# Kernel tuning notes

Measured on AMD Instinct MI355X. Metric: run time of the kernel, lower is better.

Reference implementation:

```python
import jax, jax.numpy as jnp
import numpy as np

B, S, H, L, NH, F, V, K, R = 64, 512, 256, 4, 8, 1024, 50265, 8, 25
DH = H // NH
EPS = 1e-5


def layernorm(x, g, b):
    mu = x.mean(-1, keepdims=True)
    var = ((x - mu) ** 2).mean(-1, keepdims=True)
    return (x - mu) * jax.lax.rsqrt(var + EPS) * g + b


def setup_inputs() -> dict:
    key = jax.random.key(0)
    ks = jax.random.split(key, 24)
    input_ids = jax.random.randint(ks[0], (B, S), 0, V, dtype=jnp.int64)
    # prefix attention mask with variable valid lengths (ragged sequences)
    lengths = jax.random.randint(ks[1], (B,), 16, S + 1)
    attention_mask = (jnp.arange(S)[None, :] < lengths[:, None]).astype(jnp.int32)
    sub_indices = jax.random.randint(ks[2], (B, K), 0, S, dtype=jnp.int64)
    obj_indices = jax.random.randint(ks[3], (B, K), 0, S, dtype=jnp.int64)
    sub_counts = jax.random.randint(ks[4], (B,), 0, K + 1, dtype=jnp.int32)
    obj_counts = jax.random.randint(ks[5], (B,), 0, K + 1, dtype=jnp.int32)
    sc = 0.02
    p = {
        'emb': jax.random.normal(ks[6], (V, H), jnp.float32) * sc,
        'Wqkv': jax.random.normal(ks[7], (L, H, 3 * H), jnp.float32) * sc,
        'bqkv': jnp.zeros((L, 3 * H), jnp.float32),
        'Wo': jax.random.normal(ks[8], (L, H, H), jnp.float32) * sc,
        'bo': jnp.zeros((L, H), jnp.float32),
        'ln1_g': jnp.ones((L, H), jnp.float32), 'ln1_b': jnp.zeros((L, H), jnp.float32),
        'ln2_g': jnp.ones((L, H), jnp.float32), 'ln2_b': jnp.zeros((L, H), jnp.float32),
        'W1': jax.random.normal(ks[9], (L, H, F), jnp.float32) * sc,
        'b1': jnp.zeros((L, F), jnp.float32),
        'W2': jax.random.normal(ks[10], (L, F, H), jnp.float32) * sc,
        'b2': jnp.zeros((L, H), jnp.float32),
        'lnf_g': jnp.ones((H,), jnp.float32), 'lnf_b': jnp.zeros((H,), jnp.float32),
        'mW1': jax.random.normal(ks[11], (3 * H, H), jnp.float32) * sc,
        'mb1': jnp.zeros((H,), jnp.float32),
        'mW2': jax.random.normal(ks[12], (H, R), jnp.float32) * sc,
        'mb2': jnp.zeros((R,), jnp.float32),
    }
    return dict(input_ids=input_ids, attention_mask=attention_mask,
                sub_indices=sub_indices, sub_counts=sub_counts,
                obj_indices=obj_indices, obj_counts=obj_counts, **p)


def _encoder(input_ids, attention_mask, emb, Wqkv, bqkv, Wo, bo,
             ln1_g, ln1_b, ln2_g, ln2_b, W1, b1, W2, b2, lnf_g, lnf_b):
    x = emb[input_ids]  # [B,S,H]
    kbias = jnp.where(attention_mask[:, None, None, :] > 0, 0.0, -1e9)  # mask keys
    scale = 1.0 / np.sqrt(DH)
    for l in range(L):  # small fixed layer loop
        qkv = x @ Wqkv[l] + bqkv[l]
        q, k, v = jnp.split(qkv, 3, axis=-1)
        q = q.reshape(B, S, NH, DH).transpose(0, 2, 1, 3)
        k = k.reshape(B, S, NH, DH).transpose(0, 2, 1, 3)
        v = v.reshape(B, S, NH, DH).transpose(0, 2, 1, 3)
        scores = jnp.einsum('bhqd,bhkd->bhqk', q, k) * scale + kbias
        attn = jax.nn.softmax(scores, axis=-1)
        o = jnp.einsum('bhqk,bhkd->bhqd', attn, v).transpose(0, 2, 1, 3).reshape(B, S, H)
        x = layernorm(x + o @ Wo[l] + bo[l], ln1_g[l], ln1_b[l])
        h = jax.nn.relu(x @ W1[l] + b1[l]) @ W2[l] + b2[l]
        x = layernorm(x + h, ln2_g[l], ln2_b[l])
    return layernorm(x, lnf_g, lnf_b)


def _pooled(seq, idx, counts):
    g = jnp.take_along_axis(seq, idx[:, :, None], axis=1)  # [B,K,H]
    m = (jnp.arange(K)[None, :] < counts[:, None]).astype(seq.dtype)
    s = (g * m[:, :, None]).sum(1)
    c = counts.astype(seq.dtype)[:, None]
    return jnp.where(c > 0, s / jnp.maximum(c, 1.0), 0.0)  # zeros if no indices


def reference(input_ids, attention_mask, sub_indices, sub_counts, obj_indices, obj_counts,
              emb, Wqkv, bqkv, Wo, bo, ln1_g, ln1_b, ln2_g, ln2_b,
              W1, b1, W2, b2, lnf_g, lnf_b, mW1, mb1, mW2, mb2):
    seq = _encoder(input_ids, attention_mask, emb, Wqkv, bqkv, Wo, bo,
                   ln1_g, ln1_b, ln2_g, ln2_b, W1, b1, W2, b2, lnf_g, lnf_b)
    sub = _pooled(seq, sub_indices, sub_counts)
    obj = _pooled(seq, obj_indices, obj_counts)
    mask = attention_mask.astype(seq.dtype)
    lens = mask.sum(1)[:, None]
    story = jnp.where(lens > 0, (seq * mask[:, :, None]).sum(1) / jnp.maximum(lens, 1.0),
                      seq.mean(1))
    feat = jnp.concatenate([sub, obj, story], axis=-1)  # [B,3H]
    logits = jax.nn.relu(feat @ mW1 + mb1) @ mW2 + mb2
    return logits
```

## Files before the change

kernel.cpp:

```cpp
#include <hip/hip_runtime.h>
#include <hip/hip_bf16.h>


typedef __hip_bfloat16 bf16;
typedef __attribute__((ext_vector_type(8))) short short8;
typedef __attribute__((ext_vector_type(4))) float f32x4;

#define S_LEN 512
#define H_DIM 256
#define NTOK  32768
#define QSCALE 0.25503488f

__device__ __forceinline__ void gload_lds16(const void* g, void* l) {
  __builtin_amdgcn_global_load_lds(
      (const __attribute__((address_space(1))) unsigned int*)g,
      (__attribute__((address_space(3))) unsigned int*)l, 16, 0, 0);
}

__device__ __forceinline__ unsigned short f2bu(float x) {
  bf16 t = __float2bfloat16(x);
  return *reinterpret_cast<unsigned short*>(&t);
}
__device__ __forceinline__ float bu2f(unsigned short u) {
  unsigned int x = (unsigned int)u << 16;
  return __uint_as_float(x);
}

__global__ __launch_bounds__(64) void lens_kernel(
    const int* __restrict__ amask, int* __restrict__ ntiles,
    int* __restrict__ lenb) {
  const int b = blockIdx.x, t = threadIdx.x;
  int c = 0;
#pragma unroll
  for (int i = 0; i < 8; ++i) c += amask[b * S_LEN + t + i * 64];
#pragma unroll
  for (int off = 1; off < 64; off <<= 1) c += __shfl_xor(c, off);
  if (t == 0) {
    lenb[b] = c;
    ntiles[b] = (c + 63) >> 6;
  }
}

__global__ __launch_bounds__(64) void order_kernel(
    const int* __restrict__ ntiles, int* __restrict__ ordb) {
  const int b = threadIdx.x;
  const int ntb = ntiles[b];
  int rank = 0;
  for (int j = 0; j < 64; ++j) {
    const int ntj = __shfl(ntb, j);
    rank += (ntj > ntb) || (ntj == ntb && j < b);
  }
  ordb[rank] = b;
}

__global__ __launch_bounds__(256) void tcast_kernel(
    const float* __restrict__ in, bf16* __restrict__ out, int K, int N) {
  const int l = blockIdx.z;
  in  += (size_t)l * K * N;
  out += (size_t)l * K * N;
  __shared__ float t[32][33];
  const int n0 = blockIdx.x * 32, k0 = blockIdx.y * 32;
  const int c = threadIdx.x & 31, r = threadIdx.x >> 5;
#pragma unroll
  for (int rr = r; rr < 32; rr += 8)
    t[rr][c] = in[(size_t)(k0 + rr) * N + n0 + c];
  __syncthreads();
#pragma unroll
  for (int rr = r; rr < 32; rr += 8)
    out[(size_t)(n0 + rr) * K + k0 + c] = __float2bfloat16(t[c][rr]);
}

__global__ __launch_bounds__(256) void embed_kernel(
    const int* __restrict__ ids, const float* __restrict__ emb,
    bf16* __restrict__ Xb) {
  size_t i4 = (size_t)blockIdx.x * 256 + threadIdx.x;
  int tok = (int)(i4 >> 6);
  int d4  = (int)(i4 & 63);
  float4 v = *(const float4*)&emb[(size_t)ids[tok] * H_DIM + d4 * 4];
  ushort4 pk;
  pk.x = f2bu(v.x); pk.y = f2bu(v.y); pk.z = f2bu(v.z); pk.w = f2bu(v.w);
  *(ushort4*)&Xb[i4 * 4] = pk;
}

#define SRC_CHUNK(tid_) (((tid_) & 3) ^ (((tid_) >> 3) & 3))

template<int MODE, bool RELU>
__global__ __launch_bounds__(256) void hgemm_kernel(
    const bf16* __restrict__ A, const bf16* __restrict__ Bt,
    const float* __restrict__ bias, float* __restrict__ Cf,
    bf16* __restrict__ Cb, bf16* __restrict__ Vt,
    int M, int N, int K) {
  __shared__ __align__(16) bf16 Sh[16384];
  bf16* const As0 = Sh;
  bf16* const Bs0 = Sh + 8192;
  const int tid = threadIdx.x;
  const int wv = tid >> 6, ln = tid & 63;
  const int fr = ln & 15, g4 = ln >> 4;
  const int wr = wv >> 1, wc = wv & 1;
  const int m0 = blockIdx.x * 128, n0 = blockIdx.y * 128;
  const int lr = tid >> 2;
  const int lk = SRC_CHUNK(tid) * 8;
  const int rc = (g4 ^ ((fr >> 1) & 3)) * 8;

#define STAGE_G(buf, kk) do {                                                  \
    const int kof_ = (kk) * 32;                                                \
    gload_lds16(A  + (size_t)(m0 + lr) * K + kof_ + lk,                        \
                &As0[(buf) * 4096 + wv * 512]);                                \
    gload_lds16(A  + (size_t)(m0 + 64 + lr) * K + kof_ + lk,                   \
                &As0[(buf) * 4096 + 2048 + wv * 512]);                         \
    gload_lds16(Bt + (size_t)(n0 + lr) * K + kof_ + lk,                        \
                &Bs0[(buf) * 4096 + wv * 512]);                                \
    gload_lds16(Bt + (size_t)(n0 + 64 + lr) * K + kof_ + lk,                   \
                &Bs0[(buf) * 4096 + 2048 + wv * 512]);                         \
  } while (0)

  f32x4 acc[4][4];
#pragma unroll
  for (int i = 0; i < 4; ++i)
#pragma unroll
    for (int j = 0; j < 4; ++j)
      acc[i][j] = (f32x4){0.f, 0.f, 0.f, 0.f};

  const int NT = K >> 5;
  STAGE_G(0, 0);
  __syncthreads();
  int cur = 0;
  for (int kt = 0; kt < NT; ++kt) {
    if (kt + 1 < NT) STAGE_G(cur ^ 1, kt + 1);
    short8 af[4], bfv[4];
#pragma unroll
    for (int i = 0; i < 4; ++i)
      af[i] = *(const short8*)
          &As0[cur * 4096 + (wr * 64 + i * 16 + fr) * 32 + rc];
#pragma unroll
    for (int j = 0; j < 4; ++j)
      bfv[j] = *(const short8*)
          &Bs0[cur * 4096 + (wc * 64 + j * 16 + fr) * 32 + rc];
#pragma unroll
    for (int i = 0; i < 4; ++i)
#pragma unroll
      for (int j = 0; j < 4; ++j)
        acc[i][j] = __builtin_amdgcn_mfma_f32_16x16x32_bf16(
            af[i], bfv[j], acc[i][j], 0, 0, 0);
    __syncthreads();
    cur ^= 1;
  }
#undef STAGE_G

  const bool vpath = (MODE == 2) && (n0 >= 512);
#pragma unroll
  for (int j = 0; j < 4; ++j) {
    const int nl = wc * 64 + j * 16 + fr;
    const int n = n0 + nl;
    const float bv = bias[n];
    const float sc = (MODE == 2 && n < 256) ? QSCALE : 1.0f;
#pragma unroll
    for (int i = 0; i < 4; ++i) {
      const int mlb = wr * 64 + i * 16 + g4 * 4;
#pragma unroll
      for (int r = 0; r < 4; ++r) {
        float o = acc[i][j][r] + bv;
        if (RELU) o = fmaxf(o, 0.f);
        o *= sc;
        const int ml = mlb + r;
        const int addr = vpath ? nl * 128 + (ml ^ ((nl & 7) << 3))
                               : ml * 128 + (nl ^ ((ml & 7) << 3));
        Sh[addr] = __float2bfloat16(o);
      }
    }
  }
  __syncthreads();
  if (!vpath) {
    const int ldc = (MODE == 1) ? N : 768;
#pragma unroll
    for (int p = 0; p < 8; ++p) {
      const int cid = p * 256 + tid;
      const int ml = cid >> 4, mc = cid & 15;
      const short8 v =
          *(const short8*)&Sh[ml * 128 + ((mc * 8) ^ ((ml & 7) << 3))];
      *(short8*)&Cb[(size_t)(m0 + ml) * ldc + n0 + mc * 8] = v;
    }
  } else {
    const int bb = m0 >> 9;
#pragma unroll
    for (int p = 0; p < 8; ++p) {
      const int cid = p * 256 + tid;
      const int ddl = cid >> 4, mc = cid & 15;
      const short8 v =
          *(const short8*)&Sh[ddl * 128 + ((mc * 8) ^ ((ddl & 7) << 3))];
      const int dd = (n0 - 512) + ddl;
      const int hh = dd >> 5, ddd = dd & 31;
      const int s8 = (m0 & 511) + mc * 8;
      const int ssw = (s8 & ~63) | ((s8 & 63) ^ ((ddd & 7) << 3));
      *(short8*)&Vt[(((size_t)bb * 8 + hh) * 32 + ddd) * 512 + ssw] = v;
    }
  }
}

__global__ __launch_bounds__(256) void hgemm_ln_kernel(
    const bf16* __restrict__ A, const bf16* __restrict__ Bt,
    const float* __restrict__ bias, bf16* __restrict__ Xbf,
    const float* __restrict__ g, const float* __restrict__ bt, int K) {
  __shared__ __align__(16) bf16 Sh[20480];
  bf16* const As0 = Sh;
  bf16* const Bs0 = Sh + 4096;
  float* const rsum = (float*)Sh;
  float* const rsq  = (float*)(Sh + 512);
  bf16*  const XbT  = Sh + 1024;
  const int tid = threadIdx.x;
  const int wv = tid >> 6;
  const int ln = tid & 63;
  const int fr = ln & 15, g4 = ln >> 4;
  const int m0 = blockIdx.x * 64;
  const int rc = (g4 ^ ((fr >> 1) & 3)) * 8;

#define STAGE_L(buf, kk) do {                                                  \
    const int kof_ = (kk) * 32;                                                \
    gload_lds16(A + (size_t)(m0 + (tid >> 2)) * K + kof_ +                     \
                    SRC_CHUNK(tid) * 8,                                        \
                &As0[(buf) * 2048 + wv * 512]);                                \
    _Pragma("unroll")                                                          \
    for (int e = 0; e < 4; ++e) {                                              \
      const int vt = e * 256 + tid;                                            \
      gload_lds16(Bt + (size_t)(vt >> 2) * K + kof_ + SRC_CHUNK(vt) * 8,       \
                  &Bs0[(buf) * 8192 + e * 2048 + wv * 512]);                   \
    }                                                                          \
  } while (0)

  f32x4 acc[4][4];
#pragma unroll
  for (int i = 0; i < 4; ++i)
#pragma unroll
    for (int j = 0; j < 4; ++j)
      acc[i][j] = (f32x4){0.f, 0.f, 0.f, 0.f};

  const int NT = K >> 5;
  STAGE_L(0, 0);
  __syncthreads();
  int cur = 0;
  for (int kt = 0; kt < NT; ++kt) {
    if (kt + 1 < NT) STAGE_L(cur ^ 1, kt + 1);
    short8 af[4], bfv[4];
#pragma unroll
    for (int i = 0; i < 4; ++i)
      af[i] = *(const short8*)&As0[cur * 2048 + (i * 16 + fr) * 32 + rc];
#pragma unroll
    for (int j = 0; j < 4; ++j)
      bfv[j] = *(const short8*)
          &Bs0[cur * 8192 + (wv * 64 + j * 16 + fr) * 32 + rc];
#pragma unroll
    for (int i = 0; i < 4; ++i)
#pragma unroll
      for (int j = 0; j < 4; ++j)
        acc[i][j] = __builtin_amdgcn_mfma_f32_16x16x32_bf16(
            af[i], bfv[j], acc[i][j], 0, 0, 0);
    __syncthreads();
    cur ^= 1;
  }
#undef STAGE_L

#pragma unroll
  for (int p = 0; p < 8; ++p) {
    const int seg = p * 4 + wv;
    gload_lds16(Xbf + (size_t)(m0 + seg * 2 + (ln >> 5)) * 256 +
                    (ln & 31) * 8,
                &XbT[seg * 512]);
  }
  __syncthreads();

  float gj[4], bj[4], bsj[4];
#pragma unroll
  for (int j = 0; j < 4; ++j) {
    const int n = wv * 64 + j * 16 + fr;
    gj[j] = g[n]; bj[j] = bt[n]; bsj[j] = bias[n];
  }
#pragma unroll
  for (int i = 0; i < 4; ++i) {
#pragma unroll
    for (int r = 0; r < 4; ++r) {
      const int ml = i * 16 + g4 * 4 + r;
#pragma unroll
      for (int j = 0; j < 4; ++j) {
        const int nl = wv * 64 + j * 16 + fr;
        acc[i][j][r] += bsj[j] +
            bu2f(*(const unsigned short*)&XbT[ml * 256 + nl]);
      }
    }
  }
#pragma unroll
  for (int i = 0; i < 4; ++i) {
#pragma unroll
    for (int r = 0; r < 4; ++r) {
      float sp = acc[i][0][r] + acc[i][1][r] + acc[i][2][r] + acc[i][3][r];
      float qp = acc[i][0][r] * acc[i][0][r] + acc[i][1][r] * acc[i][1][r] +
                 acc[i][2][r] * acc[i][2][r] + acc[i][3][r] * acc[i][3][r];
#pragma unroll
      for (int off = 1; off < 16; off <<= 1) {
        sp += __shfl_xor(sp, off);
        qp += __shfl_xor(qp, off);
      }
      if (fr == 0) {
        const int ri = i * 16 + g4 * 4 + r;
        rsum[wv * 64 + ri] = sp;
        rsq[wv * 64 + ri] = qp;
      }
    }
  }
  __syncthreads();
#pragma unroll
  for (int i = 0; i < 4; ++i) {
#pragma unroll
    for (int r = 0; r < 4; ++r) {
      const int ri = i * 16 + g4 * 4 + r;
      const float tot = rsum[ri] + rsum[64 + ri] + rsum[128 + ri] +
                        rsum[192 + ri];
      const float tq = rsq[ri] + rsq[64 + ri] + rsq[128 + ri] + rsq[192 + ri];
      const float mu = tot * (1.0f / 256.0f);
      const float var = tq * (1.0f / 256.0f) - mu * mu;
      const float rstd = rsqrtf(var + 1e-5f);
#pragma unroll
      for (int j = 0; j < 4; ++j) {
        const int nl = wv * 64 + j * 16 + fr;
        const float o = (acc[i][j][r] - mu) * rstd * gj[j] + bj[j];
        XbT[ri * 256 + (nl ^ ((ri & 7) << 3))] = __float2bfloat16(o);
      }
    }
  }
  __syncthreads();
#pragma unroll
  for (int p = 0; p < 8; ++p) {
    const int c8 = p * 256 + tid;
    const int row = c8 >> 5, cc = c8 & 31;
    const short8 v =
        *(const short8*)&XbT[row * 256 + ((cc * 8) ^ ((row & 7) << 3))];
    *(short8*)&Xbf[(size_t)(m0 + row) * 256 + cc * 8] = v;
  }
}

__global__ __launch_bounds__(256) void attn_mfma_kernel(
    const bf16* __restrict__ QKVb, const bf16* __restrict__ Vt,
    const int* __restrict__ amask, const int* __restrict__ ntiles,
    const int* __restrict__ ordb, bf16* __restrict__ Ob) {
  const int b = ordb[blockIdx.z];
  const int h = blockIdx.y, q0 = blockIdx.x * 64;
  const int tid = threadIdx.x;
  const int wv = tid >> 6, ln = tid & 63;
  const int fr = ln & 15, g4 = ln >> 4;
  const int f8 = (fr & 7) << 3;
  const int rc = (g4 ^ ((fr >> 1) & 3)) * 8;
  const int bh32 = (b * 8 + h) * 32;
  __shared__ __align__(16) bf16 Ks[2][2048];
  __shared__ __align__(16) bf16 Vs[2][2048];
  __shared__ __align__(16) bf16 Ps[4096];
  __shared__ __align__(16) float Ms[64];

  const int nt = ntiles[b];

#define STAGE_A(buf, kt_) do {                                                 \
    const int k0_ = (kt_) * 64;                                                \
    gload_lds16(QKVb + (size_t)(b * S_LEN + k0_ + (tid >> 2)) * 768 + 256 +    \
                    h * 32 + SRC_CHUNK(tid) * 8,                               \
                &Ks[(buf)][wv * 512]);                                         \
    gload_lds16(Vt + (size_t)(bh32 + (tid >> 3)) * 512 + k0_ + (tid & 7) * 8,  \
                &Vs[(buf)][wv * 512]);                                         \
    if ((kt_) == nt - 1 && tid < 64)                                           \
      Ms[tid] = (amask[b * S_LEN + k0_ + tid] != 0) ? 0.f : -1e9f;             \
  } while (0)

  gload_lds16(QKVb + (size_t)(b * S_LEN + q0 + (tid >> 2)) * 768 + h * 32 +
                  SRC_CHUNK(tid) * 8,
              &Ps[wv * 512]);
  STAGE_A(0, 0);
  __syncthreads();
  const short8 qb = *(const short8*)&Ps[(wv * 16 + fr) * 32 + rc];
  __syncthreads();

  f32x4 accO[2], accS;
  accO[0] = (f32x4){0.f, 0.f, 0.f, 0.f};
  accO[1] = (f32x4){0.f, 0.f, 0.f, 0.f};
  accS    = (f32x4){0.f, 0.f, 0.f, 0.f};
  short8 ones;
#pragma unroll
  for (int z = 0; z < 8; ++z) ones[z] = (short)0x3F80;
  float mrun = -1e30f;
  const int srcq = 20 * g4;

  int cur = 0;
  for (int kt = 0; kt < nt; ++kt) {
    if (kt + 1 < nt) STAGE_A(cur ^ 1, kt + 1);
    const bool bnd = (kt == nt - 1);

    f32x4 st[4];
#pragma unroll
    for (int kb = 0; kb < 4; ++kb) {
      const short8 kf = *(const short8*)&Ks[cur][(kb * 16 + fr) * 32 + rc];
      f32x4 z = (f32x4){0.f, 0.f, 0.f, 0.f};
      st[kb] = __builtin_amdgcn_mfma_f32_16x16x32_bf16(kf, qb, z, 0, 0, 0);
    }

    float p[16];
    if (bnd) {
#pragma unroll
      for (int kb = 0; kb < 4; ++kb) {
        const f32x4 mv = ((const f32x4*)Ms)[kb * 4 + g4];
#pragma unroll
        for (int rr = 0; rr < 4; ++rr) p[kb * 4 + rr] = st[kb][rr] + mv[rr];
      }
    } else {
#pragma unroll
      for (int kb = 0; kb < 4; ++kb)
#pragma unroll
        for (int rr = 0; rr < 4; ++rr) p[kb * 4 + rr] = st[kb][rr];
    }

    const float a0 = fmaxf(fmaxf(p[0], p[1]), p[2]);
    const float a1 = fmaxf(fmaxf(p[3], p[4]), p[5]);
    const float a2 = fmaxf(fmaxf(p[6], p[7]), p[8]);
    const float a3 = fmaxf(fmaxf(p[9], p[10]), p[11]);
    const float a4 = fmaxf(fmaxf(p[12], p[13]), p[14]);
    float mx = fmaxf(fmaxf(fmaxf(a0, a1), fmaxf(a2, a3)), fmaxf(a4, p[15]));
    mx = fmaxf(mx, __shfl_xor(mx, 16));
    mx = fmaxf(mx, __shfl_xor(mx, 32));

    if (!__all(mx <= mrun + 8.f)) {
      const float mnew = fmaxf(mrun, mx);
      const float corr = exp2f(mrun - mnew);
      mrun = mnew;
#pragma unroll
      for (int rr = 0; rr < 4; ++rr) {
        const float cs = __shfl(corr, srcq + rr);
        accO[0][rr] *= cs;
        accO[1][rr] *= cs;
        accS[rr]    *= cs;
      }
    }

#pragma unroll
    for (int i = 0; i < 16; ++i) p[i] = exp2f(p[i] - mrun);

#pragma unroll
    for (int kb = 0; kb < 4; ++kb) {
      ushort4 w4;
      w4.x = f2bu(p[kb * 4 + 0]);
      w4.y = f2bu(p[kb * 4 + 1]);
      w4.z = f2bu(p[kb * 4 + 2]);
      w4.w = f2bu(p[kb * 4 + 3]);
      *(ushort4*)&Ps[wv * 1024 + fr * 64 + ((kb * 16 + g4 * 4) ^ f8)] = w4;
    }

#pragma unroll
    for (int kk = 0; kk < 2; ++kk) {
      const short8 pa = *(const short8*)
          &Ps[wv * 1024 + fr * 64 + ((kk * 32 + g4 * 8) ^ f8)];
      accS = __builtin_amdgcn_mfma_f32_16x16x32_bf16(pa, ones, accS, 0, 0, 0);
#pragma unroll
      for (int df = 0; df < 2; ++df) {
        const short8 vb = *(const short8*)
            &Vs[cur][(df * 16 + fr) * 64 + ((kk * 32 + g4 * 8) ^ f8)];
        accO[df] = __builtin_amdgcn_mfma_f32_16x16x32_bf16(
            pa, vb, accO[df], 0, 0, 0);
      }
    }
    __syncthreads();
    cur ^= 1;
  }
#undef STAGE_A

#pragma unroll
  for (int rr = 0; rr < 4; ++rr) {
    const float iv = 1.0f / accS[rr];
    const int q = q0 + wv * 16 + g4 * 4 + rr;
    const size_t orow = ((size_t)b * S_LEN + q) * H_DIM + h * 32;
    Ob[orow + fr]      = __float2bfloat16(accO[0][rr] * iv);
    Ob[orow + 16 + fr] = __float2bfloat16(accO[1][rr] * iv);
  }
}

__global__ __launch_bounds__(256) void lnf_pool_kernel(
    bf16* __restrict__ Xbf, const float* __restrict__ g,
    const float* __restrict__ bt, const int* __restrict__ amask,
    float* __restrict__ Pstory) {
  const int b = blockIdx.x, sg = blockIdx.y;
  const int tid = threadIdx.x, wv = tid >> 6, ln = tid & 63;
  const float4 gg = ((const float4*)g)[ln];
  const float4 bb = ((const float4*)bt)[ln];
  float ax = 0.f, ay = 0.f, az = 0.f, aw = 0.f;
  for (int t = wv; t < 64; t += 4) {
    const size_t tok = (size_t)b * S_LEN + sg * 64 + t;
    const ushort4 u = *(const ushort4*)&Xbf[tok * 256 + ln * 4];
    const float vx = bu2f(u.x), vy = bu2f(u.y), vz = bu2f(u.z),
                vw = bu2f(u.w);
    float s = vx + vy + vz + vw;
#pragma unroll
    for (int off = 1; off < 64; off <<= 1) s += __shfl_xor(s, off);
    const float mu = s * (1.0f / 256.0f);
    const float dx = vx - mu, dy = vy - mu, dz = vz - mu, dw = vw - mu;
    float sq = dx * dx + dy * dy + dz * dz + dw * dw;
#pragma unroll
    for (int off = 1; off < 64; off <<= 1) sq += __shfl_xor(sq, off);
    const float rstd = rsqrtf(sq * (1.0f / 256.0f) + 1e-5f);
    const float ox = dx * rstd * gg.x + bb.x;
    const float oy = dy * rstd * gg.y + bb.y;
    const float oz = dz * rstd * gg.z + bb.z;
    const float ow = dw * rstd * gg.w + bb.w;
    ushort4 o4;
    o4.x = f2bu(ox); o4.y = f2bu(oy); o4.z = f2bu(oz); o4.w = f2bu(ow);
    *(ushort4*)&Xbf[tok * 256 + ln * 4] = o4;
    if (amask[tok]) { ax += ox; ay += oy; az += oz; aw += ow; }
  }
  __shared__ float part[4][256];
  part[wv][ln * 4 + 0] = ax;
  part[wv][ln * 4 + 1] = ay;
  part[wv][ln * 4 + 2] = az;
  part[wv][ln * 4 + 3] = aw;
  __syncthreads();
  const float tot = part[0][tid] + part[1][tid] + part[2][tid] + part[3][tid];
  Pstory[((size_t)b * 8 + sg) * 256 + tid] = tot;
}

__global__ __launch_bounds__(256) void poolcls_kernel(
    const bf16* __restrict__ Xbf, const float* __restrict__ Pstory,
    const int* __restrict__ lenb,
    const int* __restrict__ sub_idx, const int* __restrict__ sub_cnt,
    const int* __restrict__ obj_idx, const int* __restrict__ obj_cnt,
    const float* __restrict__ mW1, const float* __restrict__ mb1,
    const float* __restrict__ mW2, const float* __restrict__ mb2,
    float* __restrict__ out) {
  const int b = blockIdx.x, t = threadIdx.x;
  __shared__ float fs[768];
  __shared__ float hid[256];
  const bf16* xb = Xbf + (size_t)b * S_LEN * H_DIM;
  {
    float s = 0.f;
#pragma unroll
    for (int i = 0; i < 8; ++i) s += Pstory[((size_t)b * 8 + i) * 256 + t];
    fs[512 + t] = s / (float)lenb[b];
  }
  {
    const int cc = sub_cnt[b];
    float s2 = 0.f;
    for (int j = 0; j < cc; ++j)
      s2 += __bfloat162float(xb[(size_t)sub_idx[b * 8 + j] * H_DIM + t]);
    fs[t] = (cc > 0) ? s2 / (float)cc : 0.f;
  }
  {
    const int cc = obj_cnt[b];
    float s2 = 0.f;
    for (int j = 0; j < cc; ++j)
      s2 += __bfloat162float(xb[(size_t)obj_idx[b * 8 + j] * H_DIM + t]);
    fs[256 + t] = (cc > 0) ? s2 / (float)cc : 0.f;
  }
  __syncthreads();
  float acc = mb1[t];
  for (int k = 0; k < 768; ++k) acc += fs[k] * mW1[(size_t)k * 256 + t];
  hid[t] = fmaxf(acc, 0.f);
  __syncthreads();
  if (t < 25) {
    float o = mb2[t];
    for (int j = 0; j < 256; ++j) o += hid[j] * mW2[j * 25 + t];
    out[b * 25 + t] = o;
  }
}

extern "C" void kernel_launch(void* const* d_in, const int* in_sizes, int n_in,
                              void* d_out, int out_size, void* d_ws, size_t ws_size,
                              hipStream_t stream) {
  const int*   input_ids = (const int*)d_in[0];
  const int*   amask     = (const int*)d_in[1];
  const int*   sub_idx   = (const int*)d_in[2];
  const int*   sub_cnt   = (const int*)d_in[3];
  const int*   obj_idx   = (const int*)d_in[4];
  const int*   obj_cnt   = (const int*)d_in[5];
  const float* emb  = (const float*)d_in[6];
  const float* Wqkv = (const float*)d_in[7];
  const float* bqkv = (const float*)d_in[8];
  const float* Wo   = (const float*)d_in[9];
  const float* bo   = (const float*)d_in[10];
  const float* ln1g = (const float*)d_in[11];
  const float* ln1b = (const float*)d_in[12];
  const float* ln2g = (const float*)d_in[13];
  const float* ln2b = (const float*)d_in[14];
  const float* W1   = (const float*)d_in[15];
  const float* b1   = (const float*)d_in[16];
  const float* W2   = (const float*)d_in[17];
  const float* b2   = (const float*)d_in[18];
  const float* lnfg = (const float*)d_in[19];
  const float* lnfb = (const float*)d_in[20];
  const float* mW1  = (const float*)d_in[21];
  const float* mb1  = (const float*)d_in[22];
  const float* mW2  = (const float*)d_in[23];
  const float* mb2  = (const float*)d_in[24];
  float* out = (float*)d_out;

  char* w = (char*)d_ws;
  bf16*  Xb   = (bf16*)w;                          w += (size_t)NTOK * 256 * 2;
  bf16*  QKVb = (bf16*)w;                          w += (size_t)NTOK * 768 * 2;
  bf16*  Vtg  = (bf16*)w;                          w += (size_t)NTOK * 256 * 2;
  bf16*  Ob   = (bf16*)w;                          w += (size_t)NTOK * 256 * 2;
  bf16*  Wqkvt= (bf16*)w;                          w += (size_t)4 * 768 * 256 * 2;
  bf16*  Wot  = (bf16*)w;                          w += (size_t)4 * 256 * 256 * 2;
  bf16*  W1t  = (bf16*)w;                          w += (size_t)4 * 1024 * 256 * 2;
  bf16*  W2t  = (bf16*)w;                          w += (size_t)4 * 256 * 1024 * 2;
  float* Pstory = (float*)w;                       w += (size_t)64 * 8 * 256 * 4;
  int*   ntiles = (int*)w;                         w += 256;
  int*   lenb   = (int*)w;                         w += 256;
  int*   ordb   = (int*)w;                         w += 256;
  bf16*  Hb   = QKVb;

  lens_kernel<<<64, 64, 0, stream>>>(amask, ntiles, lenb);
  order_kernel<<<1, 64, 0, stream>>>(ntiles, ordb);
  tcast_kernel<<<dim3(24, 8, 4), 256, 0, stream>>>(Wqkv, Wqkvt, 256, 768);
  tcast_kernel<<<dim3(8, 8, 4), 256, 0, stream>>>(Wo, Wot, 256, 256);
  tcast_kernel<<<dim3(32, 8, 4), 256, 0, stream>>>(W1, W1t, 256, 1024);
  tcast_kernel<<<dim3(8, 32, 4), 256, 0, stream>>>(W2, W2t, 1024, 256);

  embed_kernel<<<8192, 256, 0, stream>>>(input_ids, emb, Xb);

  for (int l = 0; l < 4; ++l) {
    const bf16* Wqkvt_l = Wqkvt + (size_t)l * 768 * 256;
    const bf16* Wot_l   = Wot + (size_t)l * 256 * 256;
    const bf16* W1t_l   = W1t + (size_t)l * 1024 * 256;
    const bf16* W2t_l   = W2t + (size_t)l * 256 * 1024;

    hgemm_kernel<2, false><<<dim3(256, 6), 256, 0, stream>>>(
        Xb, Wqkvt_l, bqkv + (size_t)l * 768, nullptr, QKVb, Vtg, NTOK, 768, 256);
    attn_mfma_kernel<<<dim3(8, 8, 64), 256, 0, stream>>>(
        QKVb, Vtg, amask, ntiles, ordb, Ob);
    hgemm_ln_kernel<<<512, 256, 0, stream>>>(
        Ob, Wot_l, bo + (size_t)l * 256, Xb,
        ln1g + l * 256, ln1b + l * 256, 256);
    hgemm_kernel<1, true><<<dim3(256, 8), 256, 0, stream>>>(
        Xb, W1t_l, b1 + (size_t)l * 1024, nullptr, Hb, nullptr, NTOK, 1024, 256);
    hgemm_ln_kernel<<<512, 256, 0, stream>>>(
        Hb, W2t_l, b2 + (size_t)l * 256, Xb,
        ln2g + l * 256, ln2b + l * 256, 1024);
  }
  lnf_pool_kernel<<<dim3(64, 8), 256, 0, stream>>>(Xb, lnfg, lnfb, amask,
                                                   Pstory);
  poolcls_kernel<<<64, 256, 0, stream>>>(Xb, Pstory, lenb, sub_idx, sub_cnt,
                                         obj_idx, obj_cnt, mW1, mb1, mW2, mb2,
                                         out);
}
```

Before: 705.5 us.

## Use 128-query attention blocks and compute softmax row sums by shuffle reduction

The attention kernel now runs 512-thread blocks covering 128 query rows per head. Each staged K/V tile in LDS is shared by eight waves instead of four, roughly halving global K/V traffic per query. The softmax denominator is now a running sum built from per-lane adds and cross-lane shuffles, replacing the extra MFMA against a ones vector. In exchange the block has a larger LDS footprint and a tighter launch bound, which may limit occupancy or cause register spills, and half the threads sit idle during staging.

```diff
diff --git a/kernel.cpp b/kernel.cpp
--- a/kernel.cpp
+++ b/kernel.cpp
@@ -337,12 +337,13 @@
   }
 }
 
-__global__ __launch_bounds__(256) void attn_mfma_kernel(
+__global__ __launch_bounds__(512, 8) void attn_mfma_kernel(
     const bf16* __restrict__ QKVb, const bf16* __restrict__ Vt,
     const int* __restrict__ amask, const int* __restrict__ ntiles,
     const int* __restrict__ ordb, bf16* __restrict__ Ob) {
   const int b = ordb[blockIdx.z];
-  const int h = blockIdx.y, q0 = blockIdx.x * 64;
+  const int h = blockIdx.x;
+  const int qg = blockIdx.y;
   const int tid = threadIdx.x;
   const int wv = tid >> 6, ln = tid & 63;
   const int fr = ln & 15, g4 = ln >> 4;
@@ -351,38 +352,37 @@
   const int bh32 = (b * 8 + h) * 32;
   __shared__ __align__(16) bf16 Ks[2][2048];
   __shared__ __align__(16) bf16 Vs[2][2048];
-  __shared__ __align__(16) bf16 Ps[4096];
+  __shared__ __align__(16) bf16 Ps[8192];
   __shared__ __align__(16) float Ms[64];
 
   const int nt = ntiles[b];
 
 #define STAGE_A(buf, kt_) do {                                                 \
-    const int k0_ = (kt_) * 64;                                                \
-    gload_lds16(QKVb + (size_t)(b * S_LEN + k0_ + (tid >> 2)) * 768 + 256 +    \
-                    h * 32 + SRC_CHUNK(tid) * 8,                               \
-                &Ks[(buf)][wv * 512]);                                         \
-    gload_lds16(Vt + (size_t)(bh32 + (tid >> 3)) * 512 + k0_ + (tid & 7) * 8,  \
-                &Vs[(buf)][wv * 512]);                                         \
-    if ((kt_) == nt - 1 && tid < 64)                                           \
-      Ms[tid] = (amask[b * S_LEN + k0_ + tid] != 0) ? 0.f : -1e9f;             \
+    if (tid < 256) {                                                           \
+      const int k0_ = (kt_) * 64;                                              \
+      gload_lds16(QKVb + (size_t)(b * S_LEN + k0_ + (tid >> 2)) * 768 + 256 +  \
+                      h * 32 + SRC_CHUNK(tid) * 8,                             \
+                  &Ks[(buf)][wv * 512]);                                       \
+      gload_lds16(Vt + (size_t)(bh32 + (tid >> 3)) * 512 + k0_ +               \
+                      (tid & 7) * 8,                                           \
+                  &Vs[(buf)][wv * 512]);                                       \
+      if ((kt_) == nt - 1 && tid < 64)                                         \
+        Ms[tid] = (amask[b * S_LEN + k0_ + tid] != 0) ? 0.f : -1e9f;           \
+    }                                                                          \
   } while (0)
 
-  gload_lds16(QKVb + (size_t)(b * S_LEN + q0 + (tid >> 2)) * 768 + h * 32 +
-                  SRC_CHUNK(tid) * 8,
+  gload_lds16(QKVb + (size_t)(b * S_LEN + qg * 128 + (tid >> 2)) * 768 +
+                  h * 32 + SRC_CHUNK(tid) * 8,
               &Ps[wv * 512]);
   STAGE_A(0, 0);
   __syncthreads();
-  const short8 qb = *(const short8*)&Ps[(wv * 16 + fr) * 32 + rc];
-  __syncthreads();
-
-  f32x4 accO[2], accS;
+  const short8 qb = *(const short8*)&Ps[wv * 512 + fr * 32 + rc];
+  __syncthreads();
+
+  f32x4 accO[2];
   accO[0] = (f32x4){0.f, 0.f, 0.f, 0.f};
   accO[1] = (f32x4){0.f, 0.f, 0.f, 0.f};
-  accS    = (f32x4){0.f, 0.f, 0.f, 0.f};
-  short8 ones;
-#pragma unroll
-  for (int z = 0; z < 8; ++z) ones[z] = (short)0x3F80;
-  float mrun = -1e30f;
+  float mrun = -1e30f, lrun = 0.f;
   const int srcq = 20 * g4;
 
   int cur = 0;
@@ -422,21 +422,28 @@
     mx = fmaxf(mx, __shfl_xor(mx, 16));
     mx = fmaxf(mx, __shfl_xor(mx, 32));
 
+    float corr = 1.f;
     if (!__all(mx <= mrun + 8.f)) {
       const float mnew = fmaxf(mrun, mx);
-      const float corr = exp2f(mrun - mnew);
+      corr = exp2f(mrun - mnew);
       mrun = mnew;
 #pragma unroll
       for (int rr = 0; rr < 4; ++rr) {
         const float cs = __shfl(corr, srcq + rr);
         accO[0][rr] *= cs;
         accO[1][rr] *= cs;
-        accS[rr]    *= cs;
       }
     }
 
 #pragma unroll
     for (int i = 0; i < 16; ++i) p[i] = exp2f(p[i] - mrun);
+    const float b0 = p[0] + p[1], b1 = p[2] + p[3], b2 = p[4] + p[5],
+                b3 = p[6] + p[7], b4 = p[8] + p[9], b5 = p[10] + p[11],
+                b6 = p[12] + p[13], b7 = p[14] + p[15];
+    float ps = ((b0 + b1) + (b2 + b3)) + ((b4 + b5) + (b6 + b7));
+    ps += __shfl_xor(ps, 16);
+    ps += __shfl_xor(ps, 32);
+    lrun = lrun * corr + ps;
 
 #pragma unroll
     for (int kb = 0; kb < 4; ++kb) {
@@ -452,7 +459,6 @@
     for (int kk = 0; kk < 2; ++kk) {
       const short8 pa = *(const short8*)
           &Ps[wv * 1024 + fr * 64 + ((kk * 32 + g4 * 8) ^ f8)];
-      accS = __builtin_amdgcn_mfma_f32_16x16x32_bf16(pa, ones, accS, 0, 0, 0);
 #pragma unroll
       for (int df = 0; df < 2; ++df) {
         const short8 vb = *(const short8*)
@@ -466,10 +472,11 @@
   }
 #undef STAGE_A
 
+  const float inv = 1.0f / lrun;
 #pragma unroll
   for (int rr = 0; rr < 4; ++rr) {
-    const float iv = 1.0f / accS[rr];
-    const int q = q0 + wv * 16 + g4 * 4 + rr;
+    const float iv = __shfl(inv, srcq + rr);
+    const int q = qg * 128 + wv * 16 + g4 * 4 + rr;
     const size_t orow = ((size_t)b * S_LEN + q) * H_DIM + h * 32;
     Ob[orow + fr]      = __float2bfloat16(accO[0][rr] * iv);
     Ob[orow + 16 + fr] = __float2bfloat16(accO[1][rr] * iv);
@@ -624,7 +631,7 @@
 
     hgemm_kernel<2, false><<<dim3(256, 6), 256, 0, stream>>>(
         Xb, Wqkvt_l, bqkv + (size_t)l * 768, nullptr, QKVb, Vtg, NTOK, 768, 256);
-    attn_mfma_kernel<<<dim3(8, 8, 64), 256, 0, stream>>>(
+    attn_mfma_kernel<<<dim3(8, 4, 64), 512, 0, stream>>>(
         QKVb, Vtg, amask, ntiles, ordb, Ob);
     hgemm_ln_kernel<<<512, 256, 0, stream>>>(
         Ob, Wot_l, bo + (size_t)l * 256, Xb,
```

New measurement: 694.3 us. About the same (-1.6%).
